# Kernel tuning notes

Measured on AMD Instinct MI355X. Metric: run time of the kernel, lower is better.

## Reference

```python
import jax, jax.numpy as jnp
import numpy as np

N_NODES = 10000
N_EDGES = 160000
NUM_FEAT = 14
DIM = 256


def gat_conv(x, src, dst, W, a_s, a_d, b, concat):
    """PyG GATConv: W [H*C, F_in], a_s/a_d [H, C], edges src->dst (self-loops included)."""
    H, C = a_s.shape
    N = x.shape[0]
    h = (x @ W.T).reshape(N, H, C)                       # [N,H,C]
    alpha_src = (h * a_s).sum(-1)                        # [N,H]
    alpha_dst = (h * a_d).sum(-1)                        # [N,H]
    e = jax.nn.leaky_relu(alpha_src[src] + alpha_dst[dst], negative_slope=0.2)  # [E,H]
    emax = jax.ops.segment_max(e, dst, num_segments=N)   # [N,H]
    emax = jnp.where(jnp.isneginf(emax), 0.0, emax)
    ex = jnp.exp(e - emax[dst])
    denom = jax.ops.segment_sum(ex, dst, num_segments=N)
    coef = ex / (denom[dst] + 1e-16)                     # segment softmax over in-edges
    out = jax.ops.segment_sum(h[src] * coef[..., None], dst, num_segments=N)  # [N,H,C]
    out = out.reshape(N, H * C) if concat else out.mean(axis=1)
    return out + b


def setup_inputs() -> dict:
    key = jax.random.key(0)
    ks = jax.random.split(key, 24)
    d = DIM
    f = NUM_FEAT
    def w(k, shape, fan_in):
        return jax.random.normal(k, shape, dtype=jnp.float32) * (1.0 / np.sqrt(fan_in))
    inp = {
        "x": jax.random.normal(ks[0], (N_NODES, f), dtype=jnp.float32),
        "edge_index": jax.random.randint(ks[1], (2, N_EDGES), 0, N_NODES, dtype=jnp.int64
                                         if jax.config.jax_enable_x64 else jnp.int32),
        # conv1: 14 -> 4 heads x 256
        "W1": w(ks[2], (4 * d, f), f),
        "a1s": w(ks[3], (4, d), d), "a1d": w(ks[4], (4, d), d),
        "b1": jnp.zeros((4 * d,), jnp.float32),
        "lw1": w(ks[5], (4 * d, f), f), "lb1": jnp.zeros((4 * d,), jnp.float32),
        # conv2: 1024 -> 4 heads x 256
        "W2": w(ks[6], (4 * d, 4 * d), 4 * d),
        "a2s": w(ks[7], (4, d), d), "a2d": w(ks[8], (4, d), d),
        "b2": jnp.zeros((4 * d,), jnp.float32),
        "lw2": w(ks[9], (4 * d, 4 * d), 4 * d), "lb2": jnp.zeros((4 * d,), jnp.float32),
        # conv3: 1024 -> 6 heads x 256, mean over heads
        "W3": w(ks[10], (6 * d, 4 * d), 4 * d),
        "a3s": w(ks[11], (6, d), d), "a3d": w(ks[12], (6, d), d),
        "b3": jnp.zeros((d,), jnp.float32),
        "lw3": w(ks[13], (d, 4 * d), 4 * d), "lb3": jnp.zeros((d,), jnp.float32),
    }
    return inp


def reference(x, edge_index, W1, a1s, a1d, b1, lw1, lb1,
              W2, a2s, a2d, b2, lw2, lb2,
              W3, a3s, a3d, b3, lw3, lb3):
    N = x.shape[0]
    loops = jnp.arange(N, dtype=edge_index.dtype)
    src = jnp.concatenate([edge_index[0], loops])
    dst = jnp.concatenate([edge_index[1], loops])
    x1 = jax.nn.elu(gat_conv(x, src, dst, W1, a1s, a1d, b1, True) + x @ lw1.T + lb1)
    x2 = jax.nn.elu(gat_conv(x1, src, dst, W2, a2s, a2d, b2, True) + x1 @ lw2.T + lb2)
    x3 = gat_conv(x2, src, dst, W3, a3s, a3d, b3, False) + x2 @ lw3.T + lb3
    return x3
```

## Files before the change

kernel.cpp:

```cpp
#include <hip/hip_runtime.h>
#include <hip/hip_bf16.h>
#include <cstddef>

#define NN 10000
#define EE0 160000
#define NF 14
#define DC 256

static inline int ceildiv(int a, int b) { return (a + b - 1) / b; }

__device__ __forceinline__ float lrelu02(float x) { return fmaxf(x, 0.2f * x); }

__device__ __forceinline__ short f2bf(float f) {
    unsigned u = __float_as_uint(f);
    unsigned r = (u + 0x7FFFu + ((u >> 16) & 1u)) >> 16;
    return (short)r;
}
__device__ __forceinline__ float bf2f(short s) {
    return __uint_as_float(((unsigned)(unsigned short)s) << 16);
}

typedef __attribute__((ext_vector_type(8))) short bf16x8;
typedef __attribute__((ext_vector_type(4))) float f32x4;

#define GLDS(gaddr, laddr)                                                         \
    __builtin_amdgcn_global_load_lds(                                              \
        (__attribute__((address_space(1))) void*)(gaddr),                          \
        (__attribute__((address_space(3))) void*)(laddr), 16, 0, 0)

__global__ void count_edges_k(const int* __restrict__ ei, int* __restrict__ counts,
                              int E0, int N) {
    int e = blockIdx.x * 256 + threadIdx.x;
    int E = E0 + N;
    if (e >= E) return;
    int dst = (e < E0) ? ei[E0 + e] : (e - E0);
    atomicAdd(&counts[dst], 1);
}

__global__ __launch_bounds__(1024) void scan_k(const int* __restrict__ counts,
                                               int* __restrict__ row_off, int n) {
    __shared__ int sums[1024];
    int t = threadIdx.x;
    int chunk = (n + 1023) >> 10;
    int base = t * chunk;
    int lim = base + chunk; if (lim > n) lim = n;
    int s = 0;
    for (int i = base; i < lim; ++i) s += counts[i];
    sums[t] = s;
    __syncthreads();
    for (int off = 1; off < 1024; off <<= 1) {
        int v = (t >= off) ? sums[t - off] : 0;
        __syncthreads();
        sums[t] += v;
        __syncthreads();
    }
    int run = (t == 0) ? 0 : sums[t - 1];
    for (int i = base; i < lim; ++i) { run += counts[i]; row_off[i + 1] = run; }
    if (t == 0) row_off[0] = 0;
}

__global__ void scatter_k(const int* __restrict__ ei, const int* __restrict__ row_off,
                          int* __restrict__ cursor, int* __restrict__ csr_src,
                          int E0, int N) {
    int e = blockIdx.x * 256 + threadIdx.x;
    int E = E0 + N;
    if (e >= E) return;
    int src, dst;
    if (e < E0) { src = ei[e]; dst = ei[E0 + e]; }
    else        { src = dst = e - E0; }
    int pos = row_off[dst] + atomicAdd(&cursor[dst], 1);
    csr_src[pos] = src;
}

__global__ __launch_bounds__(256) void cvt_bf16_fused_k(
    const float* __restrict__ p0, short* __restrict__ q0, int n0,
    const float* __restrict__ p1, short* __restrict__ q1, int n1,
    const float* __restrict__ p2, short* __restrict__ q2, int n2,
    const float* __restrict__ p3, short* __restrict__ q3, int n3) {
    int i = blockIdx.x * 256 + threadIdx.x;
    const float* in; short* out; int idx;
    if (i < n0) { in = p0; out = q0; idx = i; }
    else if (i < n0 + n1) { in = p1; out = q1; idx = i - n0; }
    else if (i < n0 + n1 + n2) { in = p2; out = q2; idx = i - n0 - n1; }
    else if (i < n0 + n1 + n2 + n3) { in = p3; out = q3; idx = i - n0 - n1 - n2; }
    else return;
    float4 v = ((const float4*)in)[idx];
    short4 o;
    o.x = f2bf(v.x); o.y = f2bf(v.y); o.z = f2bf(v.z); o.w = f2bf(v.w);
    ((short4*)out)[idx] = o;
}

__global__ __launch_bounds__(256) void pad_bf16_k(
    const float* __restrict__ p0, short* __restrict__ q0, int r0,
    const float* __restrict__ p1, short* __restrict__ q1, int r1,
    const float* __restrict__ p2, short* __restrict__ q2, int r2,
    int K, int Kp) {
    int i = blockIdx.x * 256 + threadIdx.x;
    int rows = r0 + r1 + r2;
    int total = rows * Kp;
    if (i >= total) return;
    int row = i / Kp, col = i - row * Kp;
    const float* in; short* out; int r;
    if (row < r0) { in = p0; out = q0; r = row; }
    else if (row < r0 + r1) { in = p1; out = q1; r = row - r0; }
    else { in = p2; out = q2; r = row - r0 - r1; }
    out[(size_t)r * Kp + col] = (col < K) ? f2bf(in[(size_t)r * K + col]) : (short)0;
}

__global__ __launch_bounds__(256) void gemm_bf16_dual(
    const short* __restrict__ A, const short* __restrict__ B,
    const float* __restrict__ b1, const float* __restrict__ b2,
    const float* __restrict__ a_s, const float* __restrict__ a_d,
    float* __restrict__ asrc, float* __restrict__ adst,
    short* __restrict__ Cb, void* __restrict__ Cf, int lin_bf16,
    int M, int Nh, int Nf, int K, int H) {
    __shared__ short As[128 * 32];
    __shared__ short Bs[128 * 32];
    const int t = threadIdx.x;
    const int wave = t >> 6, lane = t & 63;

    const int gx = gridDim.x;
    const int nwg = gx * gridDim.y;
    const int orig = blockIdx.y * gx + blockIdx.x;
    const int xcd = orig & 7;
    const int q = nwg >> 3, rmd = nwg & 7;
    const int wgid = (xcd < rmd ? xcd * (q + 1) : rmd * (q + 1) + (xcd - rmd) * q)
                     + (orig >> 3);
    const int m0 = (wgid / gx) * 128, n0 = (wgid % gx) * 128;

    const int wm = (wave >> 1) * 64, wn = (wave & 1) * 64;
    const int lane15 = lane & 15, quad = lane >> 4;

    const int lrow = lane >> 2;
    const int lk = ((lane & 3) ^ ((lrow >> 1) & 3)) * 8;
    int arow0 = m0 + wave * 16 + lrow;
    int arow1 = arow0 + 64;
    if (arow0 > M - 1) arow0 = M - 1;
    if (arow1 > M - 1) arow1 = M - 1;
    const short* ag0 = A + (size_t)arow0 * K + lk;
    const short* ag1 = A + (size_t)arow1 * K + lk;
    const short* bg0 = B + (size_t)(n0 + wave * 16 + lrow) * K + lk;
    const short* bg1 = B + (size_t)(n0 + 64 + wave * 16 + lrow) * K + lk;
    short* al0 = &As[(wave * 16) * 32];
    short* al1 = &As[(64 + wave * 16) * 32];
    short* bl0 = &Bs[(wave * 16) * 32];
    short* bl1 = &Bs[(64 + wave * 16) * 32];

    const int rql = (quad ^ ((lane15 >> 1) & 3)) * 8;

    f32x4 acc[4][4];
#pragma unroll
    for (int i = 0; i < 4; ++i)
#pragma unroll
        for (int j = 0; j < 4; ++j) acc[i][j] = (f32x4){0.f, 0.f, 0.f, 0.f};

    for (int k0 = 0; k0 < K; k0 += 32) {
        GLDS(ag0 + k0, al0);
        GLDS(ag1 + k0, al1);
        GLDS(bg0 + k0, bl0);
        GLDS(bg1 + k0, bl1);
        __syncthreads();
        bf16x8 af[4], bfr[4];
#pragma unroll
        for (int i = 0; i < 4; ++i)
            af[i] = *(const bf16x8*)&As[(wm + 16 * i + lane15) * 32 + rql];
#pragma unroll
        for (int j = 0; j < 4; ++j)
            bfr[j] = *(const bf16x8*)&Bs[(wn + 16 * j + lane15) * 32 + rql];
#pragma unroll
        for (int i = 0; i < 4; ++i)
#pragma unroll
            for (int j = 0; j < 4; ++j)
                acc[i][j] = __builtin_amdgcn_mfma_f32_16x16x32_bf16(
                    af[i], bfr[j], acc[i][j], 0, 0, 0);
        __syncthreads();
    }

    if (n0 >= Nh) {
#pragma unroll
        for (int j = 0; j < 4; ++j) {
            int nc = n0 - Nh + wn + 16 * j + lane15;
            float bias = b1[nc] + b2[nc];
#pragma unroll
            for (int i = 0; i < 4; ++i) {
                int mb = m0 + wm + 16 * i + quad * 4;
#pragma unroll
                for (int r = 0; r < 4; ++r) {
                    int m = mb + r;
                    if (m < M) {
                        float v = acc[i][j][r] + bias;
                        if (lin_bf16) ((short*)Cf)[(size_t)m * Nf + nc] = f2bf(v);
                        else          ((float*)Cf)[(size_t)m * Nf + nc] = v;
                    }
                }
            }
        }
    } else {
        const int head = (n0 + wn) >> 8;
        const int cb = (n0 + wn) & 255;
        float asv[4], adv[4];
#pragma unroll
        for (int j = 0; j < 4; ++j) {
            asv[j] = a_s[head * DC + cb + 16 * j + lane15];
            adv[j] = a_d[head * DC + cb + 16 * j + lane15];
        }
#pragma unroll
        for (int j = 0; j < 4; ++j) {
            int n = n0 + wn + 16 * j + lane15;
#pragma unroll
            for (int i = 0; i < 4; ++i) {
                int mb = m0 + wm + 16 * i + quad * 4;
#pragma unroll
                for (int r = 0; r < 4; ++r) {
                    int m = mb + r;
                    if (m < M) Cb[(size_t)m * Nh + n] = f2bf(acc[i][j][r]);
                }
            }
        }
#pragma unroll
        for (int i = 0; i < 4; ++i) {
#pragma unroll
            for (int r = 0; r < 4; ++r) {
                float s = acc[i][0][r] * asv[0] + acc[i][1][r] * asv[1] +
                          acc[i][2][r] * asv[2] + acc[i][3][r] * asv[3];
                float d = acc[i][0][r] * adv[0] + acc[i][1][r] * adv[1] +
                          acc[i][2][r] * adv[2] + acc[i][3][r] * adv[3];
#pragma unroll
                for (int off = 8; off > 0; off >>= 1) {
                    s += __shfl_xor(s, off);
                    d += __shfl_xor(d, off);
                }
                int m = m0 + wm + 16 * i + quad * 4 + r;
                if (lane15 == 0 && m < M) {
                    atomicAdd(&asrc[(size_t)m * H + head], s);
                    atomicAdd(&adst[(size_t)m * H + head], d);
                }
            }
        }
    }
}

__global__ __launch_bounds__(256) void gat_agg(
    const short* __restrict__ hbuf, const short* __restrict__ lin,
    const float* __restrict__ asrc, const float* __restrict__ adst_a,
    const int* __restrict__ row_off, const int* __restrict__ csr_src,
    short* __restrict__ outx, int N, int H) {
    int wid = (int)((blockIdx.x * (size_t)blockDim.x + threadIdx.x) >> 6);
    int lane = threadIdx.x & 63;
    if (wid >= N * H) return;
    int n = wid / H, hh = wid - n * H;
    int beg = row_off[n], end = row_off[n + 1];
    int deg = end - beg;
    float ad = adst_a[wid];

    size_t cbase = (size_t)n * H * DC + hh * DC + lane * 4;
    const short4 lv = *(const short4*)(lin + cbase);
    float4 acc = make_float4(bf2f(lv.x), bf2f(lv.y), bf2f(lv.z), bf2f(lv.w));

    if (deg <= 64) {
        int s = 0; float e = -1e38f;
        if (lane < deg) {
            s = csr_src[beg + lane];
            e = lrelu02(asrc[s * H + hh] + ad);
        }
        float m = e;
#pragma unroll
        for (int off = 32; off > 0; off >>= 1) m = fmaxf(m, __shfl_xor(m, off));
        float p = (lane < deg) ? __expf(e - m) : 0.f;
        float dsum = p;
#pragma unroll
        for (int off = 32; off > 0; off >>= 1) dsum += __shfl_xor(dsum, off);
        float coef = p / (dsum + 1e-16f);

        const size_t hoff = (size_t)hh * DC + lane * 4;
        int i = 0;
        for (; i + 8 <= deg; i += 8) {
            short4 v[8]; float wv[8];
#pragma unroll
            for (int u = 0; u < 8; ++u) {
                int su = __shfl(s, i + u);
                v[u] = *(const short4*)(hbuf + (size_t)su * (H * DC) + hoff);
                wv[u] = __shfl(coef, i + u);
            }
#pragma unroll
            for (int u = 0; u < 8; ++u) {
                acc.x += wv[u] * bf2f(v[u].x);
                acc.y += wv[u] * bf2f(v[u].y);
                acc.z += wv[u] * bf2f(v[u].z);
                acc.w += wv[u] * bf2f(v[u].w);
            }
        }
        for (; i < deg; ++i) {
            float wv = __shfl(coef, i);
            int si = __shfl(s, i);
            const short4 hv = *(const short4*)(hbuf + (size_t)si * (H * DC) + hoff);
            acc.x += wv * bf2f(hv.x); acc.y += wv * bf2f(hv.y);
            acc.z += wv * bf2f(hv.z); acc.w += wv * bf2f(hv.w);
        }
    } else {
        float m = -1e38f;
        for (int i = beg + lane; i < end; i += 64) {
            int s = csr_src[i];
            m = fmaxf(m, lrelu02(asrc[s * H + hh] + ad));
        }
#pragma unroll
        for (int off = 32; off > 0; off >>= 1) m = fmaxf(m, __shfl_xor(m, off));
        float dsum = 0.f;
        for (int i = beg + lane; i < end; i += 64) {
            int s = csr_src[i];
            dsum += __expf(lrelu02(asrc[s * H + hh] + ad) - m);
        }
#pragma unroll
        for (int off = 32; off > 0; off >>= 1) dsum += __shfl_xor(dsum, off);
        float inv = 1.f / (dsum + 1e-16f);
        for (int i = beg; i < end; ++i) {
            int s = csr_src[i];
            float wv = __expf(lrelu02(asrc[s * H + hh] + ad) - m) * inv;
            const short4 hv = *(const short4*)(hbuf + ((size_t)s * H + hh) * DC + lane * 4);
            acc.x += wv * bf2f(hv.x); acc.y += wv * bf2f(hv.y);
            acc.z += wv * bf2f(hv.z); acc.w += wv * bf2f(hv.w);
        }
    }
    acc.x = acc.x > 0.f ? acc.x : __expf(acc.x) - 1.f;
    acc.y = acc.y > 0.f ? acc.y : __expf(acc.y) - 1.f;
    acc.z = acc.z > 0.f ? acc.z : __expf(acc.z) - 1.f;
    acc.w = acc.w > 0.f ? acc.w : __expf(acc.w) - 1.f;
    short4 o;
    o.x = f2bf(acc.x); o.y = f2bf(acc.y); o.z = f2bf(acc.z); o.w = f2bf(acc.w);
    *(short4*)(outx + cbase) = o;
}

__global__ __launch_bounds__(384) void gat_agg_mean(
    const short* __restrict__ hbuf, const float* __restrict__ asrc,
    const float* __restrict__ adst_a, const int* __restrict__ row_off,
    const int* __restrict__ csr_src, float* __restrict__ out, int N) {
    const int H = 6;
    __shared__ float red[6][DC];
    int n = blockIdx.x;
    int wave = threadIdx.x >> 6, lane = threadIdx.x & 63;
    int hh = wave;
    int beg = row_off[n], end = row_off[n + 1];
    int deg = end - beg;
    const float invH = 1.f / 6.f;
    float ad = adst_a[n * H + hh];

    float4 acc = make_float4(0.f, 0.f, 0.f, 0.f);
    const size_t hoff = (size_t)hh * DC + lane * 4;

    if (deg <= 64) {
        int s = 0; float e = -1e38f;
        if (lane < deg) {
            s = csr_src[beg + lane];
            e = lrelu02(asrc[s * H + hh] + ad);
        }
        float m = e;
#pragma unroll
        for (int off = 32; off > 0; off >>= 1) m = fmaxf(m, __shfl_xor(m, off));
        float p = (lane < deg) ? __expf(e - m) : 0.f;
        float dsum = p;
#pragma unroll
        for (int off = 32; off > 0; off >>= 1) dsum += __shfl_xor(dsum, off);
        float coef = p * invH / (dsum + 1e-16f);

        int i = 0;
        for (; i + 8 <= deg; i += 8) {
            short4 v[8]; float wv[8];
#pragma unroll
            for (int u = 0; u < 8; ++u) {
                int su = __shfl(s, i + u);
                v[u] = *(const short4*)(hbuf + (size_t)su * (H * DC) + hoff);
                wv[u] = __shfl(coef, i + u);
            }
#pragma unroll
            for (int u = 0; u < 8; ++u) {
                acc.x += wv[u] * bf2f(v[u].x);
                acc.y += wv[u] * bf2f(v[u].y);
                acc.z += wv[u] * bf2f(v[u].z);
                acc.w += wv[u] * bf2f(v[u].w);
            }
        }
        for (; i < deg; ++i) {
            float wv = __shfl(coef, i);
            int si = __shfl(s, i);
            const short4 hv = *(const short4*)(hbuf + (size_t)si * (H * DC) + hoff);
            acc.x += wv * bf2f(hv.x); acc.y += wv * bf2f(hv.y);
            acc.z += wv * bf2f(hv.z); acc.w += wv * bf2f(hv.w);
        }
    } else {
        float m = -1e38f;
        for (int i = beg + lane; i < end; i += 64) {
            int s = csr_src[i];
            m = fmaxf(m, lrelu02(asrc[s * H + hh] + ad));
        }
#pragma unroll
        for (int off = 32; off > 0; off >>= 1) m = fmaxf(m, __shfl_xor(m, off));
        float dsum = 0.f;
        for (int i = beg + lane; i < end; i += 64) {
            int s = csr_src[i];
            dsum += __expf(lrelu02(asrc[s * H + hh] + ad) - m);
        }
#pragma unroll
        for (int off = 32; off > 0; off >>= 1) dsum += __shfl_xor(dsum, off);
        float inv = invH / (dsum + 1e-16f);
        for (int i = beg; i < end; ++i) {
            int s = csr_src[i];
            float wv = __expf(lrelu02(asrc[s * H + hh] + ad) - m) * inv;
            const short4 hv = *(const short4*)(hbuf + (size_t)s * (H * DC) + hoff);
            acc.x += wv * bf2f(hv.x); acc.y += wv * bf2f(hv.y);
            acc.z += wv * bf2f(hv.z); acc.w += wv * bf2f(hv.w);
        }
    }
    *(float4*)&red[wave][lane * 4] = acc;
    __syncthreads();
    if (wave == 0) {
        float* op = out + (size_t)n * DC + lane * 4;
        float4 o = *(float4*)op;
#pragma unroll
        for (int j = 0; j < 6; ++j) {
            float4 r = *(float4*)&red[j][lane * 4];
            o.x += r.x; o.y += r.y; o.z += r.z; o.w += r.w;
        }
        *(float4*)op = o;
    }
}

extern "C" void kernel_launch(void* const* d_in, const int* in_sizes, int n_in,
                              void* d_out, int out_size, void* d_ws, size_t ws_size,
                              hipStream_t stream) {
    const float* x   = (const float*)d_in[0];
    const int*   ei  = (const int*)d_in[1];
    const float* W1  = (const float*)d_in[2];
    const float* a1s = (const float*)d_in[3];
    const float* a1d = (const float*)d_in[4];
    const float* b1  = (const float*)d_in[5];
    const float* lw1 = (const float*)d_in[6];
    const float* lb1 = (const float*)d_in[7];
    const float* W2  = (const float*)d_in[8];
    const float* a2s = (const float*)d_in[9];
    const float* a2d = (const float*)d_in[10];
    const float* b2  = (const float*)d_in[11];
    const float* lb2_w = (const float*)d_in[12];
    const float* lb2 = (const float*)d_in[13];
    const float* W3  = (const float*)d_in[14];
    const float* a3s = (const float*)d_in[15];
    const float* a3d = (const float*)d_in[16];
    const float* b3  = (const float*)d_in[17];
    const float* lw3 = (const float*)d_in[18];
    const float* lb3 = (const float*)d_in[19];
    const float* lw2 = lb2_w;
    float* out = (float*)d_out;

    const int N = NN, E0 = EE0, E = EE0 + NN;

    unsigned char* w = (unsigned char*)d_ws;
    size_t off = 0;
    auto alloc = [&](size_t bytes) {
        void* p = w + off;
        off += (bytes + 255) & ~(size_t)255;
        return p;
    };
    short* hbuf   = (short*)alloc((size_t)N * 1536 * 2);
    short* buf    = (short*)alloc((size_t)N * 1024 * 2);
    short* xb     = (short*)alloc((size_t)N * 1024 * 2);
    short* xpad   = (short*)alloc((size_t)N * 32 * 2);
    short* W1p    = (short*)alloc((size_t)1024 * 32 * 2);
    short* lw1p   = (short*)alloc((size_t)1024 * 32 * 2);
    short* W2b    = (short*)alloc((size_t)1024 * 1024 * 2);
    short* lw2b   = (short*)alloc((size_t)1024 * 1024 * 2);
    short* W3b    = (short*)alloc((size_t)1536 * 1024 * 2);
    short* lw3b   = (short*)alloc((size_t)256 * 1024 * 2);
    float* alpha  = (float*)alloc((size_t)2 * N * 6 * 4);
    float* asrc   = alpha;
    float* adst   = alpha + (size_t)N * 6;
    int* row_off  = (int*)alloc((size_t)(N + 1) * 4);
    int* counts2  = (int*)alloc((size_t)2 * N * 4);
    int* counts   = counts2;
    int* cursor   = counts2 + N;
    int* csr_src  = (int*)alloc((size_t)E * 4);
    (void)ws_size; (void)n_in; (void)in_sizes; (void)out_size;

    const size_t alpha_bytes = (size_t)2 * N * 6 * 4;

    hipMemsetAsync(counts2, 0, (size_t)2 * N * 4, stream);
    count_edges_k<<<ceildiv(E, 256), 256, 0, stream>>>(ei, counts, E0, N);
    scan_k<<<1, 1024, 0, stream>>>(counts, row_off, N);
    scatter_k<<<ceildiv(E, 256), 256, 0, stream>>>(ei, row_off, cursor, csr_src, E0, N);

    {
        int q0 = 1024 * 1024 / 4, q1 = 1024 * 1024 / 4, q2 = 1536 * 1024 / 4,
            q3 = 256 * 1024 / 4;
        cvt_bf16_fused_k<<<ceildiv(q0 + q1 + q2 + q3, 256), 256, 0, stream>>>(
            W2, W2b, q0, lw2, lw2b, q1, W3, W3b, q2, lw3, lw3b, q3);
        int rows = N + 1024 + 1024;
        pad_bf16_k<<<ceildiv(rows * 32, 256), 256, 0, stream>>>(
            x, xpad, N, W1, W1p, 1024, lw1, lw1p, 1024, NF, 32);
    }

    hipMemsetAsync(alpha, 0, alpha_bytes, stream);
    gemm_bf16_dual<<<dim3(16, ceildiv(N, 128)), 256, 0, stream>>>(
        xpad, W1p, b1, lb1, a1s, a1d, asrc, adst, hbuf, (void*)buf, 1,
        N, 1024, 1024, 32, 4);
    gat_agg<<<ceildiv(N * 4, 4), 256, 0, stream>>>(hbuf, buf, asrc, adst, row_off,
                                                   csr_src, xb, N, 4);

    hipMemsetAsync(alpha, 0, alpha_bytes, stream);
    gemm_bf16_dual<<<dim3(16, ceildiv(N, 128)), 256, 0, stream>>>(
        xb, W2b, b2, lb2, a2s, a2d, asrc, adst, hbuf, (void*)buf, 1,
        N, 1024, 1024, 1024, 4);
    gat_agg<<<ceildiv(N * 4, 4), 256, 0, stream>>>(hbuf, buf, asrc, adst, row_off,
                                                   csr_src, xb, N, 4);

    hipMemsetAsync(alpha, 0, alpha_bytes, stream);
    gemm_bf16_dual<<<dim3(14, ceildiv(N, 128)), 256, 0, stream>>>(
        xb, W3b, b3, lb3, a3s, a3d, asrc, adst, hbuf, (void*)out, 0,
        N, 1536, 256, 1024, 6);
    gat_agg_mean<<<N, 384, 0, stream>>>(hbuf, asrc, adst, row_off, csr_src, out, N);
}
```

Measured before the change: 511.6 us.

## Replace alpha atomics with per-chunk partials and reduction kernel; drop XCD remap

The GEMM epilogue no longer uses atomicAdd to accumulate per-head attention logits. Each 64-column chunk now writes its partial dot products to a dedicated buffer, and a new small kernel sums the four chunks per head. This removes the atomics and the per-layer memsets, at the cost of an extra kernel launch per layer. The XCD-aware workgroup remapping is also removed in favour of plain blockIdx tile indexing, which changes L2 locality across XCDs.

```diff
diff --git a/kernel.cpp b/kernel.cpp
--- a/kernel.cpp
+++ b/kernel.cpp
@@ -111,23 +111,14 @@
     const short* __restrict__ A, const short* __restrict__ B,
     const float* __restrict__ b1, const float* __restrict__ b2,
     const float* __restrict__ a_s, const float* __restrict__ a_d,
-    float* __restrict__ asrc, float* __restrict__ adst,
+    float* __restrict__ ps, float* __restrict__ pd,
     short* __restrict__ Cb, void* __restrict__ Cf, int lin_bf16,
     int M, int Nh, int Nf, int K, int H) {
     __shared__ short As[128 * 32];
     __shared__ short Bs[128 * 32];
     const int t = threadIdx.x;
     const int wave = t >> 6, lane = t & 63;
-
-    const int gx = gridDim.x;
-    const int nwg = gx * gridDim.y;
-    const int orig = blockIdx.y * gx + blockIdx.x;
-    const int xcd = orig & 7;
-    const int q = nwg >> 3, rmd = nwg & 7;
-    const int wgid = (xcd < rmd ? xcd * (q + 1) : rmd * (q + 1) + (xcd - rmd) * q)
-                     + (orig >> 3);
-    const int m0 = (wgid / gx) * 128, n0 = (wgid % gx) * 128;
-
+    const int m0 = blockIdx.y * 128, n0 = blockIdx.x * 128;
     const int wm = (wave >> 1) * 64, wn = (wave & 1) * 64;
     const int lane15 = lane & 15, quad = lane >> 4;
 
@@ -196,7 +187,8 @@
             }
         }
     } else {
-        const int head = (n0 + wn) >> 8;
+        const int chunk = (n0 + wn) >> 6;
+        const int head = chunk >> 2;
         const int cb = (n0 + wn) & 255;
         float asv[4], adv[4];
 #pragma unroll
@@ -217,6 +209,8 @@
                 }
             }
         }
+        float* psc = ps + (size_t)chunk * M;
+        float* pdc = pd + (size_t)chunk * M;
 #pragma unroll
         for (int i = 0; i < 4; ++i) {
 #pragma unroll
@@ -231,13 +225,26 @@
                     d += __shfl_xor(d, off);
                 }
                 int m = m0 + wm + 16 * i + quad * 4 + r;
-                if (lane15 == 0 && m < M) {
-                    atomicAdd(&asrc[(size_t)m * H + head], s);
-                    atomicAdd(&adst[(size_t)m * H + head], d);
-                }
-            }
-        }
-    }
+                if (lane15 == 0 && m < M) { psc[m] = s; pdc[m] = d; }
+            }
+        }
+    }
+}
+
+__global__ __launch_bounds__(256) void alpha_reduce_k(
+    const float* __restrict__ ps, const float* __restrict__ pd,
+    float* __restrict__ asrc, float* __restrict__ adst, int M, int H) {
+    int m = blockIdx.x * 256 + threadIdx.x;
+    int h = blockIdx.y;
+    if (m >= M) return;
+    float s = 0.f, d = 0.f;
+#pragma unroll
+    for (int c = 0; c < 4; ++c) {
+        s += ps[(size_t)(h * 4 + c) * M + m];
+        d += pd[(size_t)(h * 4 + c) * M + m];
+    }
+    asrc[m * H + h] = s;
+    adst[m * H + h] = d;
 }
 
 __global__ __launch_bounds__(256) void gat_agg(
@@ -469,17 +476,16 @@
     short* lw2b   = (short*)alloc((size_t)1024 * 1024 * 2);
     short* W3b    = (short*)alloc((size_t)1536 * 1024 * 2);
     short* lw3b   = (short*)alloc((size_t)256 * 1024 * 2);
-    float* alpha  = (float*)alloc((size_t)2 * N * 6 * 4);
-    float* asrc   = alpha;
-    float* adst   = alpha + (size_t)N * 6;
+    float* psrc   = (float*)alloc((size_t)24 * N * 4);
+    float* pdst   = (float*)alloc((size_t)24 * N * 4);
+    float* asrc   = (float*)alloc((size_t)N * 6 * 4);
+    float* adst   = (float*)alloc((size_t)N * 6 * 4);
     int* row_off  = (int*)alloc((size_t)(N + 1) * 4);
     int* counts2  = (int*)alloc((size_t)2 * N * 4);
     int* counts   = counts2;
     int* cursor   = counts2 + N;
     int* csr_src  = (int*)alloc((size_t)E * 4);
     (void)ws_size; (void)n_in; (void)in_sizes; (void)out_size;
-
-    const size_t alpha_bytes = (size_t)2 * N * 6 * 4;
 
     hipMemsetAsync(counts2, 0, (size_t)2 * N * 4, stream);
     count_edges_k<<<ceildiv(E, 256), 256, 0, stream>>>(ei, counts, E0, N);
@@ -496,23 +502,26 @@
             x, xpad, N, W1, W1p, 1024, lw1, lw1p, 1024, NF, 32);
     }
 
-    hipMemsetAsync(alpha, 0, alpha_bytes, stream);
     gemm_bf16_dual<<<dim3(16, ceildiv(N, 128)), 256, 0, stream>>>(
-        xpad, W1p, b1, lb1, a1s, a1d, asrc, adst, hbuf, (void*)buf, 1,
+        xpad, W1p, b1, lb1, a1s, a1d, psrc, pdst, hbuf, (void*)buf, 1,
         N, 1024, 1024, 32, 4);
+    alpha_reduce_k<<<dim3(ceildiv(N, 256), 4), 256, 0, stream>>>(
+        psrc, pdst, asrc, adst, N, 4);
     gat_agg<<<ceildiv(N * 4, 4), 256, 0, stream>>>(hbuf, buf, asrc, adst, row_off,
                                                    csr_src, xb, N, 4);
 
-    hipMemsetAsync(alpha, 0, alpha_bytes, stream);
     gemm_bf16_dual<<<dim3(16, ceildiv(N, 128)), 256, 0, stream>>>(
-        xb, W2b, b2, lb2, a2s, a2d, asrc, adst, hbuf, (void*)buf, 1,
+        xb, W2b, b2, lb2, a2s, a2d, psrc, pdst, hbuf, (void*)buf, 1,
         N, 1024, 1024, 1024, 4);
+    alpha_reduce_k<<<dim3(ceildiv(N, 256), 4), 256, 0, stream>>>(
+        psrc, pdst, asrc, adst, N, 4);
     gat_agg<<<ceildiv(N * 4, 4), 256, 0, stream>>>(hbuf, buf, asrc, adst, row_off,
                                                    csr_src, xb, N, 4);
 
-    hipMemsetAsync(alpha, 0, alpha_bytes, stream);
     gemm_bf16_dual<<<dim3(14, ceildiv(N, 128)), 256, 0, stream>>>(
-        xb, W3b, b3, lb3, a3s, a3d, asrc, adst, hbuf, (void*)out, 0,
+        xb, W3b, b3, lb3, a3s, a3d, psrc, pdst, hbuf, (void*)out, 0,
         N, 1536, 256, 1024, 6);
+    alpha_reduce_k<<<dim3(ceildiv(N, 256), 6), 256, 0, stream>>>(
+        psrc, pdst, asrc, adst, N, 6);
     gat_agg_mean<<<N, 384, 0, stream>>>(hbuf, asrc, adst, row_off, csr_src, out, N);
 }
```

After: 472.6 us. 7.6% less time.
